# Optimization experiments

Hardware: AMD Instinct MI355X
Metric: run time of the kernel (lower is better)

## Reference

```python
import jax, jax.numpy as jnp
import numpy as np

D_MODEL = 96
N_HEAD = 3
HEAD_DIM = D_MODEL // N_HEAD  # 32
D_FF = 2048
WIDTH = 65
HALF_W = (WIDTH - 1) // 2  # 32
EPS = 1e-5


def layer_norm(x, g, b):
    mu = jnp.mean(x, axis=-1, keepdims=True)
    var = jnp.mean(jnp.square(x - mu), axis=-1, keepdims=True)
    return (x - mu) * jax.lax.rsqrt(var + EPS) * g + b


def setup_inputs() -> dict:
    key = jax.random.key(0)
    ks = jax.random.split(key, 8)
    B, T = 8, 2048
    s = 0.05
    return {
        "x": jax.random.normal(ks[0], (B, D_MODEL, T), dtype=jnp.float32),
        "w_qkv": jax.random.normal(ks[1], (3 * D_MODEL, D_MODEL), dtype=jnp.float32) * s,
        "b_qkv": jnp.zeros((3 * D_MODEL,), dtype=jnp.float32),
        "w_out": jax.random.normal(ks[2], (D_MODEL, D_MODEL), dtype=jnp.float32) * s,
        "b_out": jnp.zeros((D_MODEL,), dtype=jnp.float32),
        "ln1_g": jnp.ones((D_MODEL,), dtype=jnp.float32),
        "ln1_b": jnp.zeros((D_MODEL,), dtype=jnp.float32),
        "w_ff1": jax.random.normal(ks[3], (D_FF, D_MODEL), dtype=jnp.float32) * s,
        "b_ff1": jnp.zeros((D_FF,), dtype=jnp.float32),
        "w_ff2": jax.random.normal(ks[4], (D_MODEL, D_FF), dtype=jnp.float32) * s,
        "b_ff2": jnp.zeros((D_MODEL,), dtype=jnp.float32),
        "ln2_g": jnp.ones((D_MODEL,), dtype=jnp.float32),
        "ln2_b": jnp.zeros((D_MODEL,), dtype=jnp.float32),
        "lnf_g": jnp.ones((D_MODEL,), dtype=jnp.float32),
        "lnf_b": jnp.zeros((D_MODEL,), dtype=jnp.float32),
    }


def reference(x, w_qkv, b_qkv, w_out, b_out, ln1_g, ln1_b, w_ff1, b_ff1,
              w_ff2, b_ff2, ln2_g, ln2_b, lnf_g, lnf_b):
    # x: (B, C, T) -> (B, T, C)
    h = jnp.transpose(x, (0, 2, 1))
    B, T, C = h.shape

    # --- multi-head self-attention with banded mask ---
    qkv = h @ w_qkv.T + b_qkv                      # (B, T, 3C)
    q, k, v = jnp.split(qkv, 3, axis=-1)
    q = q.reshape(B, T, N_HEAD, HEAD_DIM)
    k = k.reshape(B, T, N_HEAD, HEAD_DIM)
    v = v.reshape(B, T, N_HEAD, HEAD_DIM)

    scale = 1.0 / jnp.sqrt(jnp.float32(HEAD_DIM))
    scores = jnp.einsum("bthd,bshd->bhts", q, k) * scale  # (B, H, T, T)

    idx = jnp.arange(T)
    band = jnp.abs(idx[:, None] - idx[None, :]) <= HALF_W  # |i-j| <= half width
    scores = jnp.where(band[None, None], scores, jnp.float32(-jnp.inf))

    attn = jax.nn.softmax(scores, axis=-1)
    ctx = jnp.einsum("bhts,bshd->bthd", attn, v).reshape(B, T, C)
    attn_out = ctx @ w_out.T + b_out

    # --- post-norm encoder layer (dropout inactive / eval mode) ---
    h = layer_norm(h + attn_out, ln1_g, ln1_b)
    ff = jax.nn.relu(h @ w_ff1.T + b_ff1) @ w_ff2.T + b_ff2
    h = layer_norm(h + ff, ln2_g, ln2_b)

    # extra layernorm applied when width is not None
    h = layer_norm(h, lnf_g, lnf_b)

    # (B, T, C) -> (B, C, T)
    return jnp.transpose(h, (0, 2, 1))
```

## Files before the change

kernel.cpp:

```cpp
#include <hip/hip_runtime.h>
#include <hip/hip_bf16.h>

#define B 8
#define T 2048
#define C 96
#define NH 3
#define HD 32
#define FFD 2048
#define HALF_W 32
#define BT (B*T)

typedef __hip_bfloat16 bf16;
typedef __attribute__((ext_vector_type(8))) short short8;
typedef __attribute__((ext_vector_type(4))) short short4v;
typedef __attribute__((ext_vector_type(16))) float floatx16;

__device__ __forceinline__ short f2bs(float v){
    __hip_bfloat16 h = __float2bfloat16(v);
    return *reinterpret_cast<short*>(&h);
}
__device__ __forceinline__ float bs2f(short s){
    unsigned u = ((unsigned)(unsigned short)s) << 16;
    return __uint_as_float(u);
}
__device__ __forceinline__ int imin(int a, int b){ return a < b ? a : b; }
__device__ __forceinline__ int imax(int a, int b){ return a > b ? a : b; }
__device__ __forceinline__ short8 ld_b64x2(const short* p){
    short4v a = *(const short4v*)p;
    short4v b = *(const short4v*)(p + 4);
    short8 v;
    v[0]=a[0]; v[1]=a[1]; v[2]=a[2]; v[3]=a[3];
    v[4]=b[0]; v[5]=b[1]; v[6]=b[2]; v[7]=b[3];
    return v;
}

__global__ void cvtw_kernel(const float* __restrict__ wq, const float* __restrict__ wo,
                            const float* __restrict__ w1, const float* __restrict__ w2,
                            bf16* __restrict__ dst){
    int i = blockIdx.x*256 + threadIdx.x;
    if(i < 27648){
        int e = i&7, lane = (i>>3)&63, r = i>>9;
        int ks = r%6, ot = r/6;
        int o = ot*32 + (lane&31);
        int k = ks*16 + (lane>>5)*8 + e;
        dst[i] = __float2bfloat16(wq[o*96 + k]);
    } else if(i < 36864){
        int j = i - 27648;
        int e = j&7, lane = (j>>3)&63, r = j>>9;
        int ks = r%6, ct = r/6;
        int c = ct*32 + (lane&31);
        int k = ks*16 + (lane>>5)*8 + e;
        dst[i] = __float2bfloat16(wo[c*96 + k]);
    } else if(i < 233472){
        int j = i - 36864;
        int e = j&7, lane = (j>>3)&63, r = j>>9;
        int ks = r%6; r /= 6;
        int w = r%4, jt = r/4;
        int row = jt*128 + w*32 + (lane&31);
        int k = ks*16 + (lane>>5)*8 + e;
        dst[i] = __float2bfloat16(w1[row*96 + k]);
    } else if(i < 430080){
        int j = i - 233472;
        int e = j&7, lane = (j>>3)&63, r = j>>9;
        int ct = r%3; r /= 3;
        int g = r%2; r /= 2;
        int w = r%4, jt = r/4;
        int c = ct*32 + (lane&31);
        int k = jt*128 + w*32 + g*16 + (lane>>5)*8 + e;
        dst[i] = __float2bfloat16(w2[c*FFD + k]);
    }
}

__global__ __launch_bounds__(256) void qkv_kernel(
    const float* __restrict__ x, const bf16* __restrict__ wqs,
    const float* __restrict__ bias, bf16* __restrict__ qkvs){
    __shared__ float xs[96*36];
    int b  = blockIdx.x >> 6;
    int t0 = (blockIdx.x & 63) * 32;
    for(int e = threadIdx.x; e < 96*8; e += 256){
        int c = e >> 3, t4 = e & 7;
        *(float4*)(xs + c*36 + t4*4) =
            *(const float4*)(x + (size_t)b*C*T + (size_t)c*T + t0 + t4*4);
    }
    __syncthreads();
    int r0 = b*T + t0;
    const int w = threadIdx.x >> 6, lane = threadIdx.x & 63;
    const int lm = lane & 31, hq = lane >> 5;
    short8 bfr[6];
    #pragma unroll
    for(int ks = 0; ks < 6; ++ks){
        short8 v;
        #pragma unroll
        for(int i = 0; i < 8; ++i)
            v[i] = f2bs(xs[(ks*16 + hq*8 + i)*36 + lm]);
        bfr[ks] = v;
    }
    int nacc = (w == 0) ? 3 : 2;
    int ots[3] = {w, w+4, 8};
    floatx16 acc[3];
    #pragma unroll
    for(int i = 0; i < 3; ++i)
        #pragma unroll
        for(int r = 0; r < 16; ++r) acc[i][r] = 0.f;
    #pragma unroll
    for(int i = 0; i < 3; ++i){
        if(i < nacc){
            #pragma unroll
            for(int ks = 0; ks < 6; ++ks){
                short8 af = *(const short8*)((const short*)wqs
                              + (size_t)(ots[i]*6 + ks)*512 + lane*8);
                acc[i] = __builtin_amdgcn_mfma_f32_32x32x16_bf16(af, bfr[ks], acc[i], 0,0,0);
            }
        }
    }
    #pragma unroll
    for(int i = 0; i < 3; ++i){
        if(i < nacc){
            int type = ots[i]/3, hh = ots[i]%3;
            size_t rowbase = (((size_t)type*B*NH) + (size_t)b*NH + hh)*T + t0 + lm;
            #pragma unroll
            for(int q = 0; q < 4; ++q){
                float4 bv = *(const float4*)(bias + ots[i]*32 + 8*q + 4*hq);
                short4v pk;
                pk[0] = f2bs(acc[i][4*q+0] + bv.x);
                pk[1] = f2bs(acc[i][4*q+1] + bv.y);
                pk[2] = f2bs(acc[i][4*q+2] + bv.z);
                pk[3] = f2bs(acc[i][4*q+3] + bv.w);
                *(short4v*)((short*)qkvs + rowbase*32 + 8*q + 4*hq) = pk;
            }
        }
    }
}

__global__ __launch_bounds__(384) void attn_op_kernel(
    const bf16* __restrict__ qkvs, const bf16* __restrict__ wos,
    const float* __restrict__ bias, const float* __restrict__ x,
    const float* __restrict__ g1, const float* __restrict__ bb1,
    bf16* __restrict__ h1b){
    __shared__ __align__(16) short VtS[3*32*132];
    __shared__ __align__(16) short PtS[6][3200];
    __shared__ float LsS[6][32];
    __shared__ __align__(16) short ctxS[64*100];
    __shared__ float red1[2][6][32];
    const int tid = threadIdx.x;
    const int w = tid / 64, lane = tid & 63;
    const int lm = lane & 31, hq = lane >> 5;
    int b  = blockIdx.x >> 5;
    int t0 = (blockIdx.x & 31) * 64;
    const int h = w >> 1, half = w & 1;

    for(int e = tid; e < 768; e += 384){
        int hh = e / 256, rem = e & 255;
        int kp = rem >> 2, d8 = rem & 3;
        const short* vb = (const short*)qkvs + ((size_t)2*B*NH + (size_t)b*NH + hh)*T*32;
        int sa = imin(imax(t0 - 32 + 2*kp, 0), T-1);
        int sb = imin(imax(t0 - 32 + 2*kp + 1, 0), T-1);
        short8 va = *(const short8*)(vb + (size_t)sa*32 + d8*8);
        short8 v2 = *(const short8*)(vb + (size_t)sb*32 + d8*8);
        #pragma unroll
        for(int j = 0; j < 8; ++j){
            int val = (int)(unsigned short)va[j] | ((int)(unsigned short)v2[j] << 16);
            *(int*)(VtS + hh*32*132 + (d8*8 + j)*132 + 2*kp) = val;
        }
    }
    const short* qb = (const short*)qkvs + ((size_t)0*B*NH + (size_t)b*NH + h)*T*32;
    const short* kb = (const short*)qkvs + ((size_t)1*B*NH + (size_t)b*NH + h)*T*32;
    short8 qf0, qf1;
    {
        const short* qrow = qb + (size_t)(t0 + 32*half + lm)*32;
        qf0 = *(const short8*)(qrow + hq*8);
        qf1 = *(const short8*)(qrow + 16 + hq*8);
    }
    floatx16 S[3];
    #pragma unroll
    for(int sub = 0; sub < 3; ++sub){
        int srow = imin(imax(t0 + 32*half - 32 + sub*32 + lm, 0), T-1);
        const short* krow = kb + (size_t)srow*32;
        short8 kf0 = *(const short8*)(krow + hq*8);
        short8 kf1 = *(const short8*)(krow + 16 + hq*8);
        floatx16 z;
        #pragma unroll
        for(int r = 0; r < 16; ++r) z[r] = 0.f;
        z = __builtin_amdgcn_mfma_f32_32x32x16_bf16(kf0, qf0, z, 0,0,0);
        z = __builtin_amdgcn_mfma_f32_32x32x16_bf16(kf1, qf1, z, 0,0,0);
        S[sub] = z;
    }
    const float scale = 0.17677669529663687f;
    float part = 0.f;
    #pragma unroll
    for(int sub = 0; sub < 3; ++sub){
        #pragma unroll
        for(int r = 0; r < 16; ++r){
            int key_local = sub*32 + (r&3) + 8*(r>>2) + 4*hq;
            int s_glob = t0 + 32*half - 32 + key_local;
            int rel = key_local - lm;
            bool ok = (rel >= 0) && (rel <= 64) && (s_glob >= 0) && (s_glob < T);
            float p = ok ? __expf(S[sub][r]*scale) : 0.f;
            S[sub][r] = p;
            part += p;
        }
    }
    float ltot = part + __shfl_xor(part, 32);
    if(hq == 0) LsS[w][lm] = ltot;
    #pragma unroll
    for(int sub = 0; sub < 3; ++sub){
        #pragma unroll
        for(int q4 = 0; q4 < 4; ++q4){
            int kbase = sub*32 + 8*q4 + 4*hq;
            short4v pk;
            pk[0] = f2bs(S[sub][4*q4+0]);
            pk[1] = f2bs(S[sub][4*q4+1]);
            pk[2] = f2bs(S[sub][4*q4+2]);
            pk[3] = f2bs(S[sub][4*q4+3]);
            *(short4v*)(PtS[w] + lm*100 + kbase) = pk;
        }
    }
    __syncthreads();
    floatx16 O;
    #pragma unroll
    for(int r = 0; r < 16; ++r) O[r] = 0.f;
    #pragma unroll
    for(int ks = 0; ks < 6; ++ks){
        short8 pa = ld_b64x2(PtS[w] + lm*100 + ks*16 + hq*8);
        short8 vf = ld_b64x2(VtS + h*32*132 + lm*132 + 32*half + ks*16 + hq*8);
        O = __builtin_amdgcn_mfma_f32_32x32x16_bf16(pa, vf, O, 0,0,0);
    }
    #pragma unroll
    for(int r = 0; r < 16; ++r){
        int qr = (r&3) + 8*(r>>2) + 4*hq;
        float linv = 1.f / LsS[w][qr];
        ctxS[(32*half + qr)*100 + h*32 + lm] = f2bs(O[r]*linv);
    }
    __syncthreads();

    const int mh = (w >= 3) ? 1 : 0;
    const int ct = w - 3*mh;
    short8 bfr[6];
    #pragma unroll
    for(int ks = 0; ks < 6; ++ks)
        bfr[ks] = ld_b64x2(ctxS + (mh*32 + lm)*100 + ks*16 + hq*8);
    floatx16 acc;
    #pragma unroll
    for(int r = 0; r < 16; ++r) acc[r] = 0.f;
    #pragma unroll
    for(int ks = 0; ks < 6; ++ks){
        short8 af = *(const short8*)((const short*)wos
                      + (size_t)(ct*6 + ks)*512 + lane*8);
        acc = __builtin_amdgcn_mfma_f32_32x32x16_bf16(af, bfr[ks], acc, 0,0,0);
    }
    const int tloc = t0 + mh*32;
    float vals[16];
    float p1 = 0.f, p2 = 0.f;
    #pragma unroll
    for(int q = 0; q < 4; ++q){
        int c = ct*32 + 8*q + 4*hq;
        float4 bv = *(const float4*)(bias + c);
        float bva[4] = {bv.x, bv.y, bv.z, bv.w};
        #pragma unroll
        for(int r = 0; r < 4; ++r){
            float xv = x[(size_t)b*C*T + (size_t)(c + r)*T + tloc + lm];
            float v = acc[4*q+r] + bva[r] + xv;
            vals[4*q+r] = v;
            p1 += v; p2 += v*v;
        }
    }
    p1 += __shfl_xor(p1, 32);
    p2 += __shfl_xor(p2, 32);
    if(hq == 0){ red1[0][w][lm] = p1; red1[1][w][lm] = p2; }
    __syncthreads();
    float s  = red1[0][mh*3+0][lm] + red1[0][mh*3+1][lm] + red1[0][mh*3+2][lm];
    float s2 = red1[1][mh*3+0][lm] + red1[1][mh*3+1][lm] + red1[1][mh*3+2][lm];
    float mu = s * (1.0f/96.0f);
    float rstd = rsqrtf(s2*(1.0f/96.0f) - mu*mu + 1e-5f);
    int row = b*T + tloc + lm;
    #pragma unroll
    for(int q = 0; q < 4; ++q){
        int c = ct*32 + 8*q + 4*hq;
        float4 gv = *(const float4*)(g1 + c);
        float4 bv = *(const float4*)(bb1 + c);
        float ga[4] = {gv.x, gv.y, gv.z, gv.w};
        float ba[4] = {bv.x, bv.y, bv.z, bv.w};
        short4v pk;
        #pragma unroll
        for(int r = 0; r < 4; ++r)
            pk[r] = f2bs((vals[4*q+r] - mu)*rstd*ga[r] + ba[r]);
        *(short4v*)((short*)h1b + (size_t)row*96 + c) = pk;
    }
}

__global__ __launch_bounds__(256, 2) void ff_ln_kernel(
    const bf16* __restrict__ h1b,
    const bf16* __restrict__ w1s, const float* __restrict__ b1,
    const bf16* __restrict__ w2s, const float* __restrict__ b2,
    const float* __restrict__ g2, const float* __restrict__ bt2,
    const float* __restrict__ gf, const float* __restrict__ btf,
    float* __restrict__ out){
    __shared__ float redp[9*1088];
    __shared__ float zt[96*33];
    const int tid = threadIdx.x;
    const int w = tid >> 6, lane = tid & 63;
    const int lm = lane & 31, hq = lane >> 5;
    const int r0 = blockIdx.x * 32;
    short8 hf[6];
    #pragma unroll
    for(int ks = 0; ks < 6; ++ks)
        hf[ks] = *(const short8*)((const short*)h1b
                   + (size_t)(r0 + lm)*96 + ks*16 + hq*8);
    floatx16 acc2[3];
    #pragma unroll
    for(int i = 0; i < 3; ++i)
        #pragma unroll
        for(int r = 0; r < 16; ++r) acc2[i][r] = 0.f;

    const short* w1p = (const short*)w1s + (size_t)w*6*512 + lane*8;
    const short* w2p = (const short*)w2s + (size_t)w*2*3*512 + lane*8;
    short8 cw1[6];
    #pragma unroll
    for(int ks = 0; ks < 6; ++ks)
        cw1[ks] = *(const short8*)(w1p + ks*512);

    #pragma unroll
    for(int jt = 0; jt < 16; ++jt){
        const int jn = (jt + 1) & 15;
        short8 nw1[6], w2f[6];
        #pragma unroll
        for(int ks = 0; ks < 6; ++ks)
            nw1[ks] = *(const short8*)(w1p + (size_t)jn*4*6*512 + ks*512);
        #pragma unroll
        for(int g = 0; g < 2; ++g)
            #pragma unroll
            for(int ct = 0; ct < 3; ++ct)
                w2f[g*3 + ct] = *(const short8*)(w2p
                                  + ((size_t)jt*4*2*3 + g*3 + ct)*512);
        floatx16 aA, aB;
        #pragma unroll
        for(int r = 0; r < 16; ++r){ aA[r] = 0.f; aB[r] = 0.f; }
        #pragma unroll
        for(int ks = 0; ks < 3; ++ks){
            aA = __builtin_amdgcn_mfma_f32_32x32x16_bf16(cw1[2*ks],   hf[2*ks],   aA, 0,0,0);
            aB = __builtin_amdgcn_mfma_f32_32x32x16_bf16(cw1[2*ks+1], hf[2*ks+1], aB, 0,0,0);
        }
        int pk[4][2];
        #pragma unroll
        for(int q = 0; q < 4; ++q){
            float4 bv = *(const float4*)(b1 + jt*128 + w*32 + 8*q + 4*hq);
            float bva[4] = {bv.x, bv.y, bv.z, bv.w};
            short4v t;
            #pragma unroll
            for(int r = 0; r < 4; ++r){
                float v = aA[4*q+r] + aB[4*q+r] + bva[r];
                t[r] = f2bs(v > 0.f ? v : 0.f);
            }
            int2 u = *(int2*)&t;
            pk[q][0] = u.x; pk[q][1] = u.y;
        }
        #pragma unroll
        for(int g = 0; g < 2; ++g){
            int a0 = pk[2*g][0],   a1 = pk[2*g][1];
            int b0 = pk[2*g+1][0], b1v = pk[2*g+1][1];
            int ra0 = __shfl_xor(a0, 32),  ra1 = __shfl_xor(a1, 32);
            int rb0 = __shfl_xor(b0, 32),  rb1 = __shfl_xor(b1v, 32);
            int4 sfi;
            sfi.x = hq ? rb0 : a0;
            sfi.y = hq ? rb1 : a1;
            sfi.z = hq ? b0  : ra0;
            sfi.w = hq ? b1v : ra1;
            short8 sf = *(short8*)&sfi;
            #pragma unroll
            for(int ct = 0; ct < 3; ++ct)
                acc2[ct] = __builtin_amdgcn_mfma_f32_32x32x16_bf16(w2f[g*3+ct], sf, acc2[ct], 0,0,0);
        }
        #pragma unroll
        for(int ks = 0; ks < 6; ++ks) cw1[ks] = nw1[ks];
    }
    __syncthreads();
    if(w > 0){
        #pragma unroll
        for(int ct = 0; ct < 3; ++ct)
            #pragma unroll
            for(int q = 0; q < 4; ++q)
                #pragma unroll
                for(int r = 0; r < 4; ++r)
                    redp[((w-1)*3 + ct)*1088 + lane*17 + 4*q + r] = acc2[ct][4*q+r];
    }
    __syncthreads();
    if(w == 0){
        float vals[48];
        float p1 = 0.f, p2 = 0.f;
        #pragma unroll
        for(int ct = 0; ct < 3; ++ct){
            #pragma unroll
            for(int q = 0; q < 4; ++q){
                int c = ct*32 + 8*q + 4*hq;
                float4 bv = *(const float4*)(b2 + c);
                short4v hv = *(const short4v*)((const short*)h1b + (size_t)(r0 + lm)*96 + c);
                float bva[4] = {bv.x, bv.y, bv.z, bv.w};
                #pragma unroll
                for(int r = 0; r < 4; ++r){
                    float v = acc2[ct][4*q+r]
                            + redp[(0*3 + ct)*1088 + lane*17 + 4*q + r]
                            + redp[(1*3 + ct)*1088 + lane*17 + 4*q + r]
                            + redp[(2*3 + ct)*1088 + lane*17 + 4*q + r]
                            + bva[r] + bs2f(hv[r]);
                    vals[ct*16 + 4*q + r] = v;
                    p1 += v; p2 += v*v;
                }
            }
        }
        p1 += __shfl_xor(p1, 32);
        p2 += __shfl_xor(p2, 32);
        float mu = p1*(1.0f/96.0f);
        float rstd = rsqrtf(p2*(1.0f/96.0f) - mu*mu + 1e-5f);
        float q1 = 0.f, q2 = 0.f;
        #pragma unroll
        for(int ct = 0; ct < 3; ++ct){
            #pragma unroll
            for(int q = 0; q < 4; ++q){
                int c = ct*32 + 8*q + 4*hq;
                float4 gv = *(const float4*)(g2 + c);
                float4 bv = *(const float4*)(bt2 + c);
                float ga[4] = {gv.x, gv.y, gv.z, gv.w};
                float ba[4] = {bv.x, bv.y, bv.z, bv.w};
                #pragma unroll
                for(int r = 0; r < 4; ++r){
                    float y = (vals[ct*16+4*q+r] - mu)*rstd*ga[r] + ba[r];
                    vals[ct*16+4*q+r] = y;
                    q1 += y; q2 += y*y;
                }
            }
        }
        q1 += __shfl_xor(q1, 32);
        q2 += __shfl_xor(q2, 32);
        float mu2 = q1*(1.0f/96.0f);
        float rstd2 = rsqrtf(q2*(1.0f/96.0f) - mu2*mu2 + 1e-5f);
        #pragma unroll
        for(int ct = 0; ct < 3; ++ct){
            #pragma unroll
            for(int q = 0; q < 4; ++q){
                int c = ct*32 + 8*q + 4*hq;
                float4 gv = *(const float4*)(gf + c);
                float4 bv = *(const float4*)(btf + c);
                float ga[4] = {gv.x, gv.y, gv.z, gv.w};
                float ba[4] = {bv.x, bv.y, bv.z, bv.w};
                #pragma unroll
                for(int r = 0; r < 4; ++r)
                    zt[(c + r)*33 + lm] = (vals[ct*16+4*q+r] - mu2)*rstd2*ga[r] + ba[r];
            }
        }
    }
    __syncthreads();
    int bb  = r0 / T;
    int t0g = r0 % T;
    for(int e = tid; e < 96*32; e += 256){
        int c = e >> 5, tt = e & 31;
        out[(size_t)bb*C*T + (size_t)c*T + t0g + tt] = zt[c*33 + tt];
    }
}

extern "C" void kernel_launch(void* const* d_in, const int* in_sizes, int n_in,
                              void* d_out, int out_size, void* d_ws, size_t ws_size,
                              hipStream_t stream) {
    const float* x     = (const float*)d_in[0];
    const float* w_qkv = (const float*)d_in[1];
    const float* b_qkv = (const float*)d_in[2];
    const float* w_out = (const float*)d_in[3];
    const float* b_out = (const float*)d_in[4];
    const float* ln1_g = (const float*)d_in[5];
    const float* ln1_b = (const float*)d_in[6];
    const float* w_ff1 = (const float*)d_in[7];
    const float* b_ff1 = (const float*)d_in[8];
    const float* w_ff2 = (const float*)d_in[9];
    const float* b_ff2 = (const float*)d_in[10];
    const float* ln2_g = (const float*)d_in[11];
    const float* ln2_b = (const float*)d_in[12];
    const float* lnf_g = (const float*)d_in[13];
    const float* lnf_b = (const float*)d_in[14];
    float* out = (float*)d_out;

    char* wsb = (char*)d_ws;
    bf16*  qkvs  = (bf16*)wsb;
    bf16*  h1b   = (bf16*)(wsb + 9437184);
    bf16*  wts   = (bf16*)(wsb + 12582912);
    bf16*  wqs   = wts;
    bf16*  wos   = wts + 27648;
    bf16*  w1s   = wts + 36864;
    bf16*  w2s   = wts + 233472;

    cvtw_kernel   <<<1680, 256, 0, stream>>>(w_qkv, w_out, w_ff1, w_ff2, wts);
    qkv_kernel    <<<BT/32, 256, 0, stream>>>(x, wqs, b_qkv, qkvs);
    attn_op_kernel<<<B*(T/64), 384, 0, stream>>>(qkvs, wos, b_out, x,
                                                 ln1_g, ln1_b, h1b);
    ff_ln_kernel  <<<BT/32, 256, 0, stream>>>(h1b, w1s, b_ff1, w2s, b_ff2,
                                              ln2_g, ln2_b, lnf_g, lnf_b, out);
}
```

Before: 128.8 us.

## Double row tile per FF block, prefetch W2 fragments, hoist W_out loads

```diff
diff --git a/kernel.cpp b/kernel.cpp
--- a/kernel.cpp
+++ b/kernel.cpp
@@ -148,6 +148,13 @@
     int b  = blockIdx.x >> 5;
     int t0 = (blockIdx.x & 31) * 64;
     const int h = w >> 1, half = w & 1;
+    const int mh = (w >= 3) ? 1 : 0;
+    const int ct = w - 3*mh;
+
+    short8 wof[6];
+    #pragma unroll
+    for(int ks = 0; ks < 6; ++ks)
+        wof[ks] = *(const short8*)((const short*)wos + (size_t)(ct*6 + ks)*512 + lane*8);
 
     for(int e = tid; e < 768; e += 384){
         int hh = e / 256, rem = e & 255;
@@ -233,8 +240,6 @@
     }
     __syncthreads();
 
-    const int mh = (w >= 3) ? 1 : 0;
-    const int ct = w - 3*mh;
     short8 bfr[6];
     #pragma unroll
     for(int ks = 0; ks < 6; ++ks)
@@ -243,11 +248,8 @@
     #pragma unroll
     for(int r = 0; r < 16; ++r) acc[r] = 0.f;
     #pragma unroll
-    for(int ks = 0; ks < 6; ++ks){
-        short8 af = *(const short8*)((const short*)wos
-                      + (size_t)(ct*6 + ks)*512 + lane*8);
-        acc = __builtin_amdgcn_mfma_f32_32x32x16_bf16(af, bfr[ks], acc, 0,0,0);
-    }
+    for(int ks = 0; ks < 6; ++ks)
+        acc = __builtin_amdgcn_mfma_f32_32x32x16_bf16(wof[ks], bfr[ks], acc, 0,0,0);
     const int tloc = t0 + mh*32;
     float vals[16];
     float p1 = 0.f, p2 = 0.f;
@@ -288,41 +290,48 @@
     }
 }
 
-__global__ __launch_bounds__(256, 2) void ff_ln_kernel(
+__global__ __launch_bounds__(512, 2) void ff_ln_kernel(
     const bf16* __restrict__ h1b,
     const bf16* __restrict__ w1s, const float* __restrict__ b1,
     const bf16* __restrict__ w2s, const float* __restrict__ b2,
     const float* __restrict__ g2, const float* __restrict__ bt2,
     const float* __restrict__ gf, const float* __restrict__ btf,
     float* __restrict__ out){
-    __shared__ float redp[9*1088];
-    __shared__ float zt[96*33];
+    __shared__ float redp[2*3*3*1088];
+    __shared__ float zt[96*65];
     const int tid = threadIdx.x;
     const int w = tid >> 6, lane = tid & 63;
     const int lm = lane & 31, hq = lane >> 5;
-    const int r0 = blockIdx.x * 32;
+    const int mt = w & 1, w4 = w >> 1;
+    const int r0 = blockIdx.x * 64;
+    const int rr = r0 + mt*32;
     short8 hf[6];
     #pragma unroll
     for(int ks = 0; ks < 6; ++ks)
         hf[ks] = *(const short8*)((const short*)h1b
-                   + (size_t)(r0 + lm)*96 + ks*16 + hq*8);
+                   + (size_t)(rr + lm)*96 + ks*16 + hq*8);
     floatx16 acc2[3];
     #pragma unroll
     for(int i = 0; i < 3; ++i)
         #pragma unroll
         for(int r = 0; r < 16; ++r) acc2[i][r] = 0.f;
 
-    const short* w1p = (const short*)w1s + (size_t)w*6*512 + lane*8;
-    const short* w2p = (const short*)w2s + (size_t)w*2*3*512 + lane*8;
-    short8 cw1[6];
+    const short* w1p = (const short*)w1s + (size_t)w4*6*512 + lane*8;
+    const short* w2p = (const short*)w2s + (size_t)w4*2*3*512 + lane*8;
+    short8 cw1[6], cw2[6];
     #pragma unroll
     for(int ks = 0; ks < 6; ++ks)
         cw1[ks] = *(const short8*)(w1p + ks*512);
+    #pragma unroll
+    for(int g = 0; g < 2; ++g)
+        #pragma unroll
+        for(int ct = 0; ct < 3; ++ct)
+            cw2[g*3 + ct] = *(const short8*)(w2p + ((size_t)g*3 + ct)*512);
 
     #pragma unroll
     for(int jt = 0; jt < 16; ++jt){
         const int jn = (jt + 1) & 15;
-        short8 nw1[6], w2f[6];
+        short8 nw1[6], nw2[6];
         #pragma unroll
         for(int ks = 0; ks < 6; ++ks)
             nw1[ks] = *(const short8*)(w1p + (size_t)jn*4*6*512 + ks*512);
@@ -330,8 +339,7 @@
         for(int g = 0; g < 2; ++g)
             #pragma unroll
             for(int ct = 0; ct < 3; ++ct)
-                w2f[g*3 + ct] = *(const short8*)(w2p
-                                  + ((size_t)jt*4*2*3 + g*3 + ct)*512);
+                nw2[g*3 + ct] = *(const short8*)(w2p + ((size_t)jn*4*2*3 + g*3 + ct)*512);
         floatx16 aA, aB;
         #pragma unroll
         for(int r = 0; r < 16; ++r){ aA[r] = 0.f; aB[r] = 0.f; }
@@ -343,7 +351,7 @@
         int pk[4][2];
         #pragma unroll
         for(int q = 0; q < 4; ++q){
-            float4 bv = *(const float4*)(b1 + jt*128 + w*32 + 8*q + 4*hq);
+            float4 bv = *(const float4*)(b1 + jt*128 + w4*32 + 8*q + 4*hq);
             float bva[4] = {bv.x, bv.y, bv.z, bv.w};
             short4v t;
             #pragma unroll
@@ -368,23 +376,25 @@
             short8 sf = *(short8*)&sfi;
             #pragma unroll
             for(int ct = 0; ct < 3; ++ct)
-                acc2[ct] = __builtin_amdgcn_mfma_f32_32x32x16_bf16(w2f[g*3+ct], sf, acc2[ct], 0,0,0);
+                acc2[ct] = __builtin_amdgcn_mfma_f32_32x32x16_bf16(cw2[g*3+ct], sf, acc2[ct], 0,0,0);
         }
         #pragma unroll
         for(int ks = 0; ks < 6; ++ks) cw1[ks] = nw1[ks];
-    }
-    __syncthreads();
-    if(w > 0){
+        #pragma unroll
+        for(int i = 0; i < 6; ++i) cw2[i] = nw2[i];
+    }
+    __syncthreads();
+    if(w4 > 0){
         #pragma unroll
         for(int ct = 0; ct < 3; ++ct)
             #pragma unroll
             for(int q = 0; q < 4; ++q)
                 #pragma unroll
                 for(int r = 0; r < 4; ++r)
-                    redp[((w-1)*3 + ct)*1088 + lane*17 + 4*q + r] = acc2[ct][4*q+r];
-    }
-    __syncthreads();
-    if(w == 0){
+                    redp[((mt*3 + (w4-1))*3 + ct)*1088 + lane*17 + 4*q + r] = acc2[ct][4*q+r];
+    }
+    __syncthreads();
+    if(w4 == 0){
         float vals[48];
         float p1 = 0.f, p2 = 0.f;
         #pragma unroll
@@ -393,14 +403,14 @@
             for(int q = 0; q < 4; ++q){
                 int c = ct*32 + 8*q + 4*hq;
                 float4 bv = *(const float4*)(b2 + c);
-                short4v hv = *(const short4v*)((const short*)h1b + (size_t)(r0 + lm)*96 + c);
+                short4v hv = *(const short4v*)((const short*)h1b + (size_t)(rr + lm)*96 + c);
                 float bva[4] = {bv.x, bv.y, bv.z, bv.w};
                 #pragma unroll
                 for(int r = 0; r < 4; ++r){
                     float v = acc2[ct][4*q+r]
-                            + redp[(0*3 + ct)*1088 + lane*17 + 4*q + r]
-                            + redp[(1*3 + ct)*1088 + lane*17 + 4*q + r]
-                            + redp[(2*3 + ct)*1088 + lane*17 + 4*q + r]
+                            + redp[((mt*3 + 0)*3 + ct)*1088 + lane*17 + 4*q + r]
+                            + redp[((mt*3 + 1)*3 + ct)*1088 + lane*17 + 4*q + r]
+                            + redp[((mt*3 + 2)*3 + ct)*1088 + lane*17 + 4*q + r]
                             + bva[r] + bs2f(hv[r]);
                     vals[ct*16 + 4*q + r] = v;
                     p1 += v; p2 += v*v;
@@ -444,16 +454,16 @@
                 float ba[4] = {bv.x, bv.y, bv.z, bv.w};
                 #pragma unroll
                 for(int r = 0; r < 4; ++r)
-                    zt[(c + r)*33 + lm] = (vals[ct*16+4*q+r] - mu2)*rstd2*ga[r] + ba[r];
+                    zt[(c + r)*65 + mt*32 + lm] = (vals[ct*16+4*q+r] - mu2)*rstd2*ga[r] + ba[r];
             }
         }
     }
     __syncthreads();
     int bb  = r0 / T;
     int t0g = r0 % T;
-    for(int e = tid; e < 96*32; e += 256){
-        int c = e >> 5, tt = e & 31;
-        out[(size_t)bb*C*T + (size_t)c*T + t0g + tt] = zt[c*33 + tt];
+    for(int e = tid; e < 96*64; e += 512){
+        int c = e >> 6, tt = e & 63;
+        out[(size_t)bb*C*T + (size_t)c*T + t0g + tt] = zt[c*65 + tt];
     }
 }
 
@@ -490,6 +500,6 @@
     qkv_kernel    <<<BT/32, 256, 0, stream>>>(x, wqs, b_qkv, qkvs);
     attn_op_kernel<<<B*(T/64), 384, 0, stream>>>(qkvs, wos, b_out, x,
                                                  ln1_g, ln1_b, h1b);
-    ff_ln_kernel  <<<BT/32, 256, 0, stream>>>(h1b, w1s, b_ff1, w2s, b_ff2,
+    ff_ln_kernel  <<<BT/64, 512, 0, stream>>>(h1b, w1s, b_ff1, w2s, b_ff2,
                                               ln2_g, ln2_b, lnf_g, lnf_b, out);
 }
```

New measurement: 126.6 us. About the same (-1.7%).
